# Performance work log

Measured on AMD Instinct MI355X. Metric: run time of the kernel, lower is better.

The kernel has to match this reference:

```python
import jax, jax.numpy as jnp
import numpy as np

NUM_HEADS = 16
HIDDEN = 1024
HEADSIZE = HIDDEN // NUM_HEADS


def setup_inputs() -> dict:
    key = jax.random.key(0)
    ks = jax.random.split(key, 9)
    B, S, H = 4, 2048, HIDDEN
    s = 1.0 / np.sqrt(H)
    return {
        "x": jax.random.normal(ks[0], (B, S, H), dtype=jnp.float32),
        "Wq": jax.random.normal(ks[1], (H, H), dtype=jnp.float32) * s,
        "bq": jax.random.normal(ks[2], (H,), dtype=jnp.float32) * s,
        "Wk": jax.random.normal(ks[3], (H, H), dtype=jnp.float32) * s,
        "bk": jax.random.normal(ks[4], (H,), dtype=jnp.float32) * s,
        "Wv": jax.random.normal(ks[5], (H, H), dtype=jnp.float32) * s,
        "bv": jax.random.normal(ks[6], (H,), dtype=jnp.float32) * s,
        "Wo": jax.random.normal(ks[7], (H, H), dtype=jnp.float32) * s,
        "bo": jax.random.normal(ks[8], (H,), dtype=jnp.float32) * s,
    }


def reference(x, Wq, bq, Wk, bk, Wv, bv, Wo, bo):
    B, S, H = x.shape
    nh, hs = NUM_HEADS, HEADSIZE

    def split_heads(y):  # (B,S,H) -> (B,nh,S,hs)
        return y.reshape(B, S, nh, hs).transpose(0, 2, 1, 3)

    q = split_heads(x @ Wq.T + bq)
    k = split_heads(x @ Wk.T + bk)
    v = split_heads(x @ Wv.T + bv)

    scores = jnp.einsum("bhqd,bhkd->bhqk", q, k) / jnp.sqrt(jnp.float32(hs))
    # causal mask: q_ind < k_ind gets -1e9 (matches torch.where(mask, -1e9, scores))
    q_ind = jnp.arange(S)[:, None]
    k_ind = jnp.arange(S)[None, :]
    scores = jnp.where(q_ind < k_ind, jnp.float32(-1e9), scores)
    attn = jax.nn.softmax(scores, axis=-1)
    out = jnp.einsum("bhqk,bhkd->bhqd", attn, v)  # (B,nh,S,hs)
    out = out.transpose(0, 2, 1, 3).reshape(B, S, H)
    return out @ Wo.T + bo
```

## Files before the change

kernel.cpp:

```cpp
#include <hip/hip_runtime.h>

#define NH 16
#define HS 64
#define HID 1024
#define SEQ 2048
#define BB 4
#define MR (BB*SEQ)
#define KD 1024
#define NT 32
#define QSCALE 0.18033688f

typedef __bf16 bf16;
typedef __attribute__((ext_vector_type(8))) __bf16 bf16x8;
typedef __attribute__((ext_vector_type(4))) __bf16 bf16x4;
typedef __attribute__((ext_vector_type(4))) float f32x4;
typedef __attribute__((ext_vector_type(16))) float f32x16;
typedef __attribute__((ext_vector_type(4))) float f4;
typedef __attribute__((ext_vector_type(2))) unsigned uintx2;

typedef __attribute__((address_space(3))) unsigned int as3u;
typedef __attribute__((address_space(1))) unsigned int as1u;

__device__ __forceinline__ void gl_lds16(const void* g, void* l) {
  __builtin_amdgcn_global_load_lds((const as1u*)g, (as3u*)l, 16, 0, 0);
}

__device__ __forceinline__ f32x4 mfma16(bf16x8 a, bf16x8 b, f32x4 c) {
  return __builtin_amdgcn_mfma_f32_16x16x32_bf16(a, b, c, 0, 0, 0);
}

__device__ __forceinline__ f32x16 mfma32(bf16x8 a, bf16x8 b, f32x16 c) {
  return __builtin_amdgcn_mfma_f32_32x32x16_bf16(a, b, c, 0, 0, 0);
}

__device__ __forceinline__ uintx2 plswap(unsigned a, unsigned b) {
#if __has_builtin(__builtin_amdgcn_permlane32_swap)
  return __builtin_amdgcn_permlane32_swap(a, b, false, false);
#else
  asm volatile("v_permlane32_swap_b32 %0, %1" : "+&v"(a), "+v"(b));
  uintx2 r; r[0] = a; r[1] = b; return r;
#endif
}

__device__ __forceinline__ float xmax32(float x) {
  uintx2 r = plswap(__float_as_uint(x), __float_as_uint(x));
  return fmaxf(__uint_as_float(r[0]), __uint_as_float(r[1]));
}
__device__ __forceinline__ float xadd32(float x) {
  uintx2 r = plswap(__float_as_uint(x), __float_as_uint(x));
  return __uint_as_float(r[0]) + __uint_as_float(r[1]);
}

__device__ __forceinline__ unsigned cvtpk(float lo, float hi) {
  unsigned r;
  asm("v_cvt_pk_bf16_f32 %0, %1, %2" : "=v"(r) : "v"(lo), "v"(hi));
  return r;
}

#define XN4   (MR*HID/4)
#define WN4   (HID*KD/4)
__global__ __launch_bounds__(256) void k_cvt_all(const float* __restrict__ x,
                                                 const float* __restrict__ w0, const float* __restrict__ w1,
                                                 const float* __restrict__ w2, const float* __restrict__ w3,
                                                 bf16* __restrict__ xb,
                                                 bf16* __restrict__ o0, bf16* __restrict__ o1,
                                                 bf16* __restrict__ o2, bf16* __restrict__ o3) {
  int i = blockIdx.x * 256 + threadIdx.x;
  const float* in; bf16* out; int j;
  if (i < XN4)            { in = x;  out = xb; j = i; }
  else if (i < XN4+WN4)   { in = w0; out = o0; j = i - XN4; }
  else if (i < XN4+2*WN4) { in = w1; out = o1; j = i - XN4 - WN4; }
  else if (i < XN4+3*WN4) { in = w2; out = o2; j = i - XN4 - 2*WN4; }
  else                    { in = w3; out = o3; j = i - XN4 - 3*WN4; }
  f4 v = reinterpret_cast<const f4*>(in)[j];
  bf16x4 h;
  h[0] = (bf16)v[0]; h[1] = (bf16)v[1]; h[2] = (bf16)v[2]; h[3] = (bf16)v[3];
  reinterpret_cast<bf16x4*>(out)[j] = h;
}

template<int MODE>
__global__ __launch_bounds__(512, 4) void k_gemm_p(const bf16* __restrict__ A,
                                                   const bf16* __restrict__ w0, const bf16* __restrict__ w1,
                                                   const bf16* __restrict__ w2,
                                                   const float* __restrict__ b0, const float* __restrict__ b1,
                                                   const float* __restrict__ b2p,
                                                   void* __restrict__ o0, void* __restrict__ o1,
                                                   void* __restrict__ o2) {
  __shared__ __align__(16) bf16 As[3][128*32];
  __shared__ __align__(16) bf16 Bs[3][256*32];
  const int tid = threadIdx.x, l = tid & 63, w = tid >> 6;
  const int wr = w >> 2, wc = w & 3;
  const int m0 = blockIdx.x * 128;
  const int ny = blockIdx.y;
  const int which = (MODE == 0) ? (ny >> 2) : 0;
  const int n0 = (MODE == 0) ? (ny & 3) * 256 : ny * 256;
  const bf16* Bw = (MODE == 1) ? w0 : (which == 0 ? w0 : which == 1 ? w1 : w2);
  const float* bias = (MODE == 1) ? b0 : (which == 0 ? b0 : which == 1 ? b1 : b2p);

  const int sra = tid >> 2;
  const int sca = (tid & 3) ^ ((sra >> 1) & 3);
  const bf16* Ag = A  + (size_t)(m0 + sra) * KD + sca * 8;
  const bf16* Bg = Bw + (size_t)(n0 + sra) * KD + sca * 8;

  gl_lds16(Ag,                        (char*)As[0] + w * 1024);
  gl_lds16(Bg,                        (char*)Bs[0] + w * 1024);
  gl_lds16(Bg + (size_t)128 * KD,     (char*)Bs[0] + 8192 + w * 1024);
  gl_lds16(Ag + 32,                   (char*)As[1] + w * 1024);
  gl_lds16(Bg + 32,                   (char*)Bs[1] + w * 1024);
  gl_lds16(Bg + (size_t)128 * KD + 32, (char*)Bs[1] + 8192 + w * 1024);

  f32x4 acc[4][4] = {};
  const int la = l & 15, lg = l >> 4;

  for (int t = 0; t < NT; ++t) {
    const int bq = t % 3;
    if (t < NT - 1) { asm volatile("s_waitcnt vmcnt(3)" ::: "memory"); }
    else            { asm volatile("s_waitcnt vmcnt(0)" ::: "memory"); }
    __builtin_amdgcn_sched_barrier(0);
    __builtin_amdgcn_s_barrier();
    __builtin_amdgcn_sched_barrier(0);

    bf16x8 af[4], bf_[2];
    #pragma unroll
    for (int mf = 0; mf < 4; mf++) {
      const int ra = wr * 64 + mf * 16 + la;
      const int ca = lg ^ ((ra >> 1) & 3);
      af[mf] = *(const bf16x8*)((const char*)As[bq] + ra * 64 + ca * 16);
    }
    #pragma unroll
    for (int nf = 0; nf < 2; nf++) {
      const int rb = wc * 64 + nf * 16 + la;
      const int cb = lg ^ ((rb >> 1) & 3);
      bf_[nf] = *(const bf16x8*)((const char*)Bs[bq] + rb * 64 + cb * 16);
    }
    const int t2 = t + 2;
    if (t2 < NT) {
      const int b2 = t2 % 3;
      gl_lds16(Ag + t2 * 32, (char*)As[b2] + w * 1024);
      gl_lds16(Bg + t2 * 32, (char*)Bs[b2] + w * 1024);
    }
    asm volatile("s_waitcnt lgkmcnt(0)" ::: "memory");
    __builtin_amdgcn_sched_barrier(0);
    __builtin_amdgcn_s_setprio(1);
    #pragma unroll
    for (int mf = 0; mf < 4; mf++) {
      acc[mf][0] = mfma16(af[mf], bf_[0], acc[mf][0]);
      acc[mf][1] = mfma16(af[mf], bf_[1], acc[mf][1]);
    }
    __builtin_amdgcn_s_setprio(0);

    #pragma unroll
    for (int nf = 0; nf < 2; nf++) {
      const int rb = wc * 64 + (nf + 2) * 16 + la;
      const int cb = lg ^ ((rb >> 1) & 3);
      bf_[nf] = *(const bf16x8*)((const char*)Bs[bq] + rb * 64 + cb * 16);
    }
    if (t2 < NT) {
      const int b2 = t2 % 3;
      gl_lds16(Bg + (size_t)128 * KD + t2 * 32, (char*)Bs[b2] + 8192 + w * 1024);
    }
    asm volatile("s_waitcnt lgkmcnt(0)" ::: "memory");
    __builtin_amdgcn_sched_barrier(0);
    __builtin_amdgcn_s_setprio(1);
    #pragma unroll
    for (int mf = 0; mf < 4; mf++) {
      acc[mf][2] = mfma16(af[mf], bf_[0], acc[mf][2]);
      acc[mf][3] = mfma16(af[mf], bf_[1], acc[mf][3]);
    }
    __builtin_amdgcn_s_setprio(0);
  }

  const float scale = (MODE == 0 && which == 0) ? QSCALE : 1.0f;
  #pragma unroll
  for (int mf = 0; mf < 4; mf++) {
    #pragma unroll
    for (int nf = 0; nf < 4; nf++) {
      const int n = n0 + wc * 64 + nf * 16 + la;
      const float bn = bias[n];
      #pragma unroll
      for (int j = 0; j < 4; j++) {
        const int m = m0 + wr * 64 + mf * 16 + lg * 4 + j;
        const float v = (acc[mf][nf][j] + bn) * scale;
        if (MODE == 0) {
          if (which == 2) {
            ((bf16*)o2)[(((size_t)(m >> 11) * NH + (n >> 6)) * HS + (n & 63)) * SEQ + (m & (SEQ - 1))] = (bf16)v;
          } else {
            bf16* dst = (which == 0) ? (bf16*)o0 : (bf16*)o1;
            dst[(((size_t)(m >> 11) * NH + (n >> 6)) * SEQ + (m & (SEQ - 1))) * HS + (n & 63)] = (bf16)v;
          }
        } else {
          ((float*)o0)[(size_t)m * HID + n] = v;
        }
      }
    }
  }
}

__global__ __launch_bounds__(256, 3) void k_attn(const bf16* __restrict__ Q,
                                                 const bf16* __restrict__ K,
                                                 const bf16* __restrict__ Vt,
                                                 bf16* __restrict__ Aout) {
  const int bh = blockIdx.x;
  const int bx = blockIdx.y;
  const int tid = threadIdx.x, l = tid & 63, w = tid >> 6;
  const int hi = l >> 5;

  __shared__ __align__(16) bf16 Ks[3][64*64];
  __shared__ __align__(16) bf16 Vs[3][64*64];

  const bf16* Qg = Q  + (size_t)bh * SEQ * HS;
  const bf16* Kg = K  + (size_t)bh * SEQ * HS;
  const bf16* Vg = Vt + (size_t)bh * HS * SEQ;

  const int bb = bh >> 4, hh = bh & 15;
  const int sr  = tid >> 3;
  const int swz = ((tid & 7) ^ (sr & 7)) * 8;

  for (int pass = 0; pass < 2; ++pass) {
    const int p_ = pass ? (15 - bx) : bx;
    const int q0 = p_ * 128;
    const int nt = 2 * p_ + 2;

    bf16x8 qf[4];
    {
      const bf16* qrow = Qg + (size_t)(q0 + w*32 + (l & 31)) * HS + hi * 8;
      #pragma unroll
      for (int m = 0; m < 4; m++)
        qf[m] = *(const bf16x8*)(qrow + m * 16);
    }
    __builtin_amdgcn_sched_barrier(0);

    #pragma unroll
    for (int i = 0; i < 2; i++) {
      gl_lds16(Kg + (size_t)(32*i + sr) * HS + swz,  (char*)Ks[0] + i*4096 + w*1024);
      gl_lds16(Vg + (size_t)(32*i + sr) * SEQ + swz, (char*)Vs[0] + i*4096 + w*1024);
    }
    #pragma unroll
    for (int i = 0; i < 2; i++) {
      gl_lds16(Kg + (size_t)(64 + 32*i + sr) * HS + swz,  (char*)Ks[1] + i*4096 + w*1024);
      gl_lds16(Vg + (size_t)(32*i + sr) * SEQ + 64 + swz, (char*)Vs[1] + i*4096 + w*1024);
    }
    asm volatile("s_waitcnt vmcnt(4)" ::: "memory");
    __builtin_amdgcn_sched_barrier(0);
    __builtin_amdgcn_s_barrier();
    __builtin_amdgcn_sched_barrier(0);

    float m_r = -1e30f, l_r = 0.f;
    f32x16 o[2] = {};
    const int qmax = q0 + w*32 + 31;
    const int qg   = q0 + w*32 + (l & 31);

    int cur = 0;
    for (int kt = 0; kt < nt; ++kt) {
      const int k0 = kt * 64;

      if (kt + 2 < nt) {
        const int k2 = k0 + 128;
        const int b2 = (cur == 0) ? 2 : cur - 1;
        #pragma unroll
        for (int i = 0; i < 2; i++) {
          gl_lds16(Kg + (size_t)(k2 + 32*i + sr) * HS + swz,  (char*)Ks[b2] + i*4096 + w*1024);
          gl_lds16(Vg + (size_t)(32*i + sr) * SEQ + k2 + swz, (char*)Vs[b2] + i*4096 + w*1024);
        }
      }

      if (k0 <= qmax) {
        f32x16 p[2] = {};
        #pragma unroll
        for (int b = 0; b < 2; b++) {
          #pragma unroll
          for (int m = 0; m < 4; m++) {
            const int row = 32*b + (l & 31);
            const int cc = 2*m + hi;
            bf16x8 kf = *(const bf16x8*)((const char*)Ks[cur] + row*128 + ((cc ^ (row & 7))*16));
            p[b] = mfma32(kf, qf[m], p[b]);
          }
        }

        if (k0 + 63 > q0 + w*32) {
          #pragma unroll
          for (int b = 0; b < 2; b++)
            #pragma unroll
            for (int r = 0; r < 16; r++) {
              const int kg = k0 + 32*b + (r & 3) + 8*(r >> 2) + 4*hi;
              if (kg > qg) p[b][r] = -1e30f;
            }
        }

        float rloc = -1e30f;
        #pragma unroll
        for (int b = 0; b < 2; b++)
          #pragma unroll
          for (int r = 0; r < 16; r++) rloc = fmaxf(rloc, p[b][r]);
        const float rmax = xmax32(rloc);

        if (__any(rmax > m_r + 8.0f)) {
          const float mn = fmaxf(m_r, rmax);
          const float alpha = __builtin_amdgcn_exp2f(m_r - mn);
          m_r = mn;
          l_r *= alpha;
          #pragma unroll
          for (int r = 0; r < 16; r++) {
            const float ar = __shfl(alpha, (r & 3) + 8*(r >> 2) + 4*hi);
            o[0][r] *= ar; o[1][r] *= ar;
          }
        }

        float sloc = 0.f;
        #pragma unroll
        for (int b = 0; b < 2; b++)
          #pragma unroll
          for (int r = 0; r < 16; r++) {
            const float e = __builtin_amdgcn_exp2f(p[b][r] - m_r);
            p[b][r] = e;
            sloc += e;
          }
        l_r += xadd32(sloc);

        bf16x8 pa[4];
        #pragma unroll
        for (int c = 0; c < 4; c++) {
          const int b = c >> 1, R = (c & 1) * 8;
          unsigned w01 = cvtpk(p[b][R+0], p[b][R+1]);
          unsigned w23 = cvtpk(p[b][R+2], p[b][R+3]);
          unsigned w89 = cvtpk(p[b][R+4], p[b][R+5]);
          unsigned wab = cvtpk(p[b][R+6], p[b][R+7]);
          uintx2 s1 = plswap(w01, w89);
          uintx2 s2 = plswap(w23, wab);
          union { unsigned u[4]; bf16x8 v; } uu;
          uu.u[0] = s1[0]; uu.u[1] = s2[0]; uu.u[2] = s1[1]; uu.u[3] = s2[1];
          pa[c] = uu.v;
        }

        #pragma unroll
        for (int d = 0; d < 2; d++) {
          #pragma unroll
          for (int c = 0; c < 4; c++) {
            const int row = 32*d + (l & 31);
            const int cc = 2*c + hi;
            bf16x8 vf = *(const bf16x8*)((const char*)Vs[cur] + row*128 + ((cc ^ (row & 7))*16));
            o[d] = mfma32(pa[c], vf, o[d]);
          }
        }
      }

      if (kt + 2 < nt) { asm volatile("s_waitcnt vmcnt(4)" ::: "memory"); }
      else             { asm volatile("s_waitcnt vmcnt(0)" ::: "memory"); }
      __builtin_amdgcn_sched_barrier(0);
      __builtin_amdgcn_s_barrier();
      __builtin_amdgcn_sched_barrier(0);
      cur = (cur == 2) ? 0 : cur + 1;
    }

    const float inv = 1.0f / l_r;
    #pragma unroll
    for (int r = 0; r < 16; r++) {
      const int qr = (r & 3) + 8*(r >> 2) + 4*hi;
      const float ir = __shfl(inv, qr);
      const int q = q0 + w*32 + qr;
      #pragma unroll
      for (int d = 0; d < 2; d++)
        Aout[(size_t)(bb*SEQ + q)*HID + hh*HS + d*32 + (l & 31)] = (bf16)(o[d][r] * ir);
    }
  }
}

extern "C" void kernel_launch(void* const* d_in, const int* in_sizes, int n_in,
                              void* d_out, int out_size, void* d_ws, size_t ws_size,
                              hipStream_t stream) {
  const float* x  = (const float*)d_in[0];
  const float* Wq = (const float*)d_in[1];
  const float* bq = (const float*)d_in[2];
  const float* Wk = (const float*)d_in[3];
  const float* bk = (const float*)d_in[4];
  const float* Wv = (const float*)d_in[5];
  const float* bv = (const float*)d_in[6];
  const float* Wo = (const float*)d_in[7];
  const float* bo = (const float*)d_in[8];

  char* ws = (char*)d_ws;
  const size_t MB = 1024 * 1024;
  bf16* xb  = (bf16*)(ws);
  bf16* wqb = (bf16*)(ws + 16*MB);
  bf16* wkb = (bf16*)(ws + 18*MB);
  bf16* wvb = (bf16*)(ws + 20*MB);
  bf16* wob = (bf16*)(ws + 22*MB);
  bf16* Qb  = (bf16*)(ws + 24*MB);
  bf16* Kb  = (bf16*)(ws + 40*MB);
  bf16* Vb  = (bf16*)(ws + 56*MB);
  bf16* Ab  = xb;

  k_cvt_all<<<(XN4 + 4*WN4 + 255)/256, 256, 0, stream>>>(x, Wq, Wk, Wv, Wo, xb, wqb, wkb, wvb, wob);

  k_gemm_p<0><<<dim3(MR/128, 12), 512, 0, stream>>>(xb, wqb, wkb, wvb, bq, bk, bv, Qb, Kb, Vb);

  k_attn<<<dim3(BB*NH, 8), 256, 0, stream>>>(Qb, Kb, Vb, Ab);

  k_gemm_p<1><<<dim3(MR/128, 4), 512, 0, stream>>>(Ab, wob, wob, wob, bo, bo, bo, d_out, d_out, d_out);
}
```

Measured before the change: 170.8 us.

## Use 256x256 ping-pong tiled QKV GEMM and smaller-tile output projection GEMM

Result: slower. 184.6 us (+8.1%).

```diff
diff --git a/kernel.cpp b/kernel.cpp
--- a/kernel.cpp
+++ b/kernel.cpp
@@ -8,6 +8,7 @@
 #define MR (BB*SEQ)
 #define KD 1024
 #define NT 32
+#define NKT 16
 #define QSCALE 0.18033688f
 
 typedef __bf16 bf16;
@@ -78,24 +79,152 @@
   reinterpret_cast<bf16x4*>(out)[j] = h;
 }
 
-template<int MODE>
-__global__ __launch_bounds__(512, 4) void k_gemm_p(const bf16* __restrict__ A,
-                                                   const bf16* __restrict__ w0, const bf16* __restrict__ w1,
-                                                   const bf16* __restrict__ w2,
-                                                   const float* __restrict__ b0, const float* __restrict__ b1,
-                                                   const float* __restrict__ b2p,
-                                                   void* __restrict__ o0, void* __restrict__ o1,
-                                                   void* __restrict__ o2) {
+extern "C" __global__ __launch_bounds__(512, 1) void k_gemm_q256(
+    const bf16* __restrict__ A, const bf16* __restrict__ w0, const bf16* __restrict__ w1,
+    const bf16* __restrict__ w2,
+    const float* __restrict__ b0, const float* __restrict__ b1, const float* __restrict__ b2p,
+    bf16* __restrict__ o0, bf16* __restrict__ o1, bf16* __restrict__ o2) {
+  extern __shared__ __align__(16) char smem[];
+  char* AsB = smem;
+  char* BsB = smem + 65536;
+  const int tid = threadIdx.x, l = tid & 63, w = tid >> 6;
+  const int wm = w >> 2, wn = w & 3;
+  const int la = l & 15, lg = l >> 4;
+  const int m0 = blockIdx.x * 256;
+  const int ny = blockIdx.y, which = ny >> 2, n0 = (ny & 3) * 256;
+  const bf16* Bw = (which == 0) ? w0 : (which == 1) ? w1 : w2;
+  const float* bias = (which == 0) ? b0 : (which == 1) ? b1 : b2p;
+
+  const int u = tid >> 3;
+  const int cg = (tid & 7) ^ (u & 7);
+
+#define SA(par, h, kt) { \
+  gl_lds16(A + (size_t)(m0 + 0*128 + (h)*64 + u) * KD + (kt)*64 + cg*8, AsB + ((par)*2+(h))*16384 + 0*8192 + tid*16); \
+  gl_lds16(A + (size_t)(m0 + 1*128 + (h)*64 + u) * KD + (kt)*64 + cg*8, AsB + ((par)*2+(h))*16384 + 1*8192 + tid*16); }
+#define SB(par, h, kt) { \
+  gl_lds16(Bw + (size_t)(n0 + 0*128 + (u>>5)*64 + (h)*32 + (u&31)) * KD + (kt)*64 + cg*8, BsB + ((par)*2+(h))*16384 + 0*8192 + tid*16); \
+  gl_lds16(Bw + (size_t)(n0 + 1*128 + (u>>5)*64 + (h)*32 + (u&31)) * KD + (kt)*64 + cg*8, BsB + ((par)*2+(h))*16384 + 1*8192 + tid*16); }
+#define RA(dst, par, mh, mf, ks) { \
+  const int r_ = wm*64 + (mf)*16 + la; const int ch_ = ((ks)*4+lg) ^ (r_ & 7); \
+  dst = *(const bf16x8*)(AsB + ((par)*2+(mh))*16384 + r_*128 + ch_*16); }
+#define RB(dst, par, nh, nf, ks) { \
+  const int r_ = wn*32 + (nf)*16 + la; const int ch_ = ((ks)*4+lg) ^ (r_ & 7); \
+  dst = *(const bf16x8*)(BsB + ((par)*2+(nh))*16384 + r_*128 + ch_*16); }
+#define SBAR __builtin_amdgcn_sched_barrier(0)
+#define BARRIER __builtin_amdgcn_s_barrier()
+#define LGKM0 asm volatile("s_waitcnt lgkmcnt(0)" ::: "memory")
+
+  SB(0, 0, 0); SA(0, 0, 0); SB(0, 1, 0); SA(0, 1, 0);
+  SB(1, 0, 1); SA(1, 0, 1);
+  asm volatile("s_waitcnt vmcnt(4)" ::: "memory");
+  SBAR; BARRIER; SBAR;
+
+  f32x4 acc[8][4] = {};
+  bf16x8 af0[4][2], af1[4][2], bf0[2][2], bf1[2][2];
+
+  for (int T = 0; T < NKT; ++T) {
+    const int par = T & 1, np = par ^ 1;
+
+    #pragma unroll
+    for (int mf = 0; mf < 4; mf++) { RA(af0[mf][0], par, 0, mf, 0); RA(af0[mf][1], par, 0, mf, 1); }
+    #pragma unroll
+    for (int nf = 0; nf < 2; nf++) { RB(bf0[nf][0], par, 0, nf, 0); RB(bf0[nf][1], par, 0, nf, 1); }
+    if (T + 1 < NKT) SB(np, 1, T + 1);
+    SBAR; BARRIER; LGKM0; SBAR;
+    __builtin_amdgcn_s_setprio(1);
+    #pragma unroll
+    for (int f = 0; f < 4; f++)
+      #pragma unroll
+      for (int g = 0; g < 2; g++)
+        #pragma unroll
+        for (int ks = 0; ks < 2; ks++)
+          acc[f][g] = mfma16(af0[f][ks], bf0[g][ks], acc[f][g]);
+    __builtin_amdgcn_s_setprio(0);
+    SBAR; BARRIER;
+
+    #pragma unroll
+    for (int mf = 0; mf < 4; mf++) { RA(af1[mf][0], par, 1, mf, 0); RA(af1[mf][1], par, 1, mf, 1); }
+    if (T + 1 < NKT) SA(np, 1, T + 1);
+    SBAR; BARRIER; LGKM0; SBAR;
+    __builtin_amdgcn_s_setprio(1);
+    #pragma unroll
+    for (int f = 0; f < 4; f++)
+      #pragma unroll
+      for (int g = 0; g < 2; g++)
+        #pragma unroll
+        for (int ks = 0; ks < 2; ks++)
+          acc[4 + f][g] = mfma16(af1[f][ks], bf0[g][ks], acc[4 + f][g]);
+    __builtin_amdgcn_s_setprio(0);
+    SBAR; BARRIER;
+
+    #pragma unroll
+    for (int nf = 0; nf < 2; nf++) { RB(bf1[nf][0], par, 1, nf, 0); RB(bf1[nf][1], par, 1, nf, 1); }
+    if (T + 2 < NKT) SB(par, 0, T + 2);
+    SBAR; BARRIER; LGKM0; SBAR;
+    __builtin_amdgcn_s_setprio(1);
+    #pragma unroll
+    for (int f = 0; f < 4; f++)
+      #pragma unroll
+      for (int g = 0; g < 2; g++)
+        #pragma unroll
+        for (int ks = 0; ks < 2; ks++)
+          acc[f][2 + g] = mfma16(af0[f][ks], bf1[g][ks], acc[f][2 + g]);
+    __builtin_amdgcn_s_setprio(0);
+    SBAR; BARRIER;
+
+    if (T + 2 < NKT) SA(par, 0, T + 2);
+    SBAR; BARRIER; SBAR;
+    __builtin_amdgcn_s_setprio(1);
+    #pragma unroll
+    for (int f = 0; f < 4; f++)
+      #pragma unroll
+      for (int g = 0; g < 2; g++)
+        #pragma unroll
+        for (int ks = 0; ks < 2; ks++)
+          acc[4 + f][2 + g] = mfma16(af1[f][ks], bf1[g][ks], acc[4 + f][2 + g]);
+    __builtin_amdgcn_s_setprio(0);
+    SBAR;
+    if (T <= NKT - 4) { asm volatile("s_waitcnt vmcnt(4)" ::: "memory"); }
+    else              { asm volatile("s_waitcnt vmcnt(0)" ::: "memory"); }
+    SBAR; BARRIER;
+  }
+#undef SA
+#undef SB
+#undef RA
+#undef RB
+
+  const float scale = (which == 0) ? QSCALE : 1.0f;
+  #pragma unroll
+  for (int mf = 0; mf < 8; mf++) {
+    #pragma unroll
+    for (int nf = 0; nf < 4; nf++) {
+      const int n = n0 + wn * 64 + (nf >> 1) * 32 + (nf & 1) * 16 + la;
+      const float bn = bias[n];
+      #pragma unroll
+      for (int j = 0; j < 4; j++) {
+        const int m = m0 + wm * 128 + (mf >> 2) * 64 + (mf & 3) * 16 + lg * 4 + j;
+        const float v = (acc[mf][nf][j] + bn) * scale;
+        if (which == 2) {
+          o2[(((size_t)(m >> 11) * NH + (n >> 6)) * HS + (n & 63)) * SEQ + (m & (SEQ - 1))] = (bf16)v;
+        } else {
+          bf16* dst = (which == 0) ? o0 : o1;
+          dst[(((size_t)(m >> 11) * NH + (n >> 6)) * SEQ + (m & (SEQ - 1))) * HS + (n & 63)] = (bf16)v;
+        }
+      }
+    }
+  }
+}
+
+__global__ __launch_bounds__(256, 3) void k_gemm_o(const bf16* __restrict__ A,
+                                                   const bf16* __restrict__ Bw,
+                                                   const float* __restrict__ bias,
+                                                   float* __restrict__ outp) {
   __shared__ __align__(16) bf16 As[3][128*32];
-  __shared__ __align__(16) bf16 Bs[3][256*32];
+  __shared__ __align__(16) bf16 Bs[3][128*32];
   const int tid = threadIdx.x, l = tid & 63, w = tid >> 6;
-  const int wr = w >> 2, wc = w & 3;
+  const int wr = w >> 1, wc = w & 1;
   const int m0 = blockIdx.x * 128;
-  const int ny = blockIdx.y;
-  const int which = (MODE == 0) ? (ny >> 2) : 0;
-  const int n0 = (MODE == 0) ? (ny & 3) * 256 : ny * 256;
-  const bf16* Bw = (MODE == 1) ? w0 : (which == 0 ? w0 : which == 1 ? w1 : w2);
-  const float* bias = (MODE == 1) ? b0 : (which == 0 ? b0 : which == 1 ? b1 : b2p);
+  const int n0 = blockIdx.y * 128;
 
   const int sra = tid >> 2;
   const int sca = (tid & 3) ^ ((sra >> 1) & 3);
@@ -103,18 +232,20 @@
   const bf16* Bg = Bw + (size_t)(n0 + sra) * KD + sca * 8;
 
   gl_lds16(Ag,                        (char*)As[0] + w * 1024);
+  gl_lds16(Ag + (size_t)64 * KD,      (char*)As[0] + 4096 + w * 1024);
   gl_lds16(Bg,                        (char*)Bs[0] + w * 1024);
-  gl_lds16(Bg + (size_t)128 * KD,     (char*)Bs[0] + 8192 + w * 1024);
+  gl_lds16(Bg + (size_t)64 * KD,      (char*)Bs[0] + 4096 + w * 1024);
   gl_lds16(Ag + 32,                   (char*)As[1] + w * 1024);
+  gl_lds16(Ag + (size_t)64 * KD + 32, (char*)As[1] + 4096 + w * 1024);
   gl_lds16(Bg + 32,                   (char*)Bs[1] + w * 1024);
-  gl_lds16(Bg + (size_t)128 * KD + 32, (char*)Bs[1] + 8192 + w * 1024);
+  gl_lds16(Bg + (size_t)64 * KD + 32, (char*)Bs[1] + 4096 + w * 1024);
 
   f32x4 acc[4][4] = {};
   const int la = l & 15, lg = l >> 4;
 
   for (int t = 0; t < NT; ++t) {
     const int bq = t % 3;
-    if (t < NT - 1) { asm volatile("s_waitcnt vmcnt(3)" ::: "memory"); }
+    if (t < NT - 1) { asm volatile("s_waitcnt vmcnt(4)" ::: "memory"); }
     else            { asm volatile("s_waitcnt vmcnt(0)" ::: "memory"); }
     __builtin_amdgcn_sched_barrier(0);
     __builtin_amdgcn_s_barrier();
@@ -136,8 +267,8 @@
     const int t2 = t + 2;
     if (t2 < NT) {
       const int b2 = t2 % 3;
-      gl_lds16(Ag + t2 * 32, (char*)As[b2] + w * 1024);
-      gl_lds16(Bg + t2 * 32, (char*)Bs[b2] + w * 1024);
+      gl_lds16(Ag + t2 * 32,                   (char*)As[b2] + w * 1024);
+      gl_lds16(Ag + (size_t)64 * KD + t2 * 32, (char*)As[b2] + 4096 + w * 1024);
     }
     asm volatile("s_waitcnt lgkmcnt(0)" ::: "memory");
     __builtin_amdgcn_sched_barrier(0);
@@ -157,7 +288,8 @@
     }
     if (t2 < NT) {
       const int b2 = t2 % 3;
-      gl_lds16(Bg + (size_t)128 * KD + t2 * 32, (char*)Bs[b2] + 8192 + w * 1024);
+      gl_lds16(Bg + t2 * 32,                   (char*)Bs[b2] + w * 1024);
+      gl_lds16(Bg + (size_t)64 * KD + t2 * 32, (char*)Bs[b2] + 4096 + w * 1024);
     }
     asm volatile("s_waitcnt lgkmcnt(0)" ::: "memory");
     __builtin_amdgcn_sched_barrier(0);
@@ -170,7 +302,6 @@
     __builtin_amdgcn_s_setprio(0);
   }
 
-  const float scale = (MODE == 0 && which == 0) ? QSCALE : 1.0f;
   #pragma unroll
   for (int mf = 0; mf < 4; mf++) {
     #pragma unroll
@@ -180,17 +311,7 @@
       #pragma unroll
       for (int j = 0; j < 4; j++) {
         const int m = m0 + wr * 64 + mf * 16 + lg * 4 + j;
-        const float v = (acc[mf][nf][j] + bn) * scale;
-        if (MODE == 0) {
-          if (which == 2) {
-            ((bf16*)o2)[(((size_t)(m >> 11) * NH + (n >> 6)) * HS + (n & 63)) * SEQ + (m & (SEQ - 1))] = (bf16)v;
-          } else {
-            bf16* dst = (which == 0) ? (bf16*)o0 : (bf16*)o1;
-            dst[(((size_t)(m >> 11) * NH + (n >> 6)) * SEQ + (m & (SEQ - 1))) * HS + (n & 63)] = (bf16)v;
-          }
-        } else {
-          ((float*)o0)[(size_t)m * HID + n] = v;
-        }
+        outp[(size_t)m * HID + n] = acc[mf][nf][j] + bn;
       }
     }
   }
@@ -390,11 +511,14 @@
   bf16* Vb  = (bf16*)(ws + 56*MB);
   bf16* Ab  = xb;
 
+  (void)hipFuncSetAttribute((const void*)k_gemm_q256,
+                            hipFuncAttributeMaxDynamicSharedMemorySize, 131072);
+
   k_cvt_all<<<(XN4 + 4*WN4 + 255)/256, 256, 0, stream>>>(x, Wq, Wk, Wv, Wo, xb, wqb, wkb, wvb, wob);
 
-  k_gemm_p<0><<<dim3(MR/128, 12), 512, 0, stream>>>(xb, wqb, wkb, wvb, bq, bk, bv, Qb, Kb, Vb);
+  k_gemm_q256<<<dim3(MR/256, 12), 512, 131072, stream>>>(xb, wqb, wkb, wvb, bq, bk, bv, Qb, Kb, Vb);
 
   k_attn<<<dim3(BB*NH, 8), 256, 0, stream>>>(Qb, Kb, Vb, Ab);
 
-  k_gemm_p<1><<<dim3(MR/128, 4), 512, 0, stream>>>(Ab, wob, wob, wob, bo, bo, bo, d_out, d_out, d_out);
-}
+  k_gemm_o<<<dim3(MR/128, 8), 256, 0, stream>>>(Ab, wob, bo, (float*)d_out);
+}
```
